# Kernel optimization log

Hardware: AMD Instinct MI355X
Metric: run time of the kernel (lower is better)

## Reference

```python
import jax, jax.numpy as jnp
import numpy as np

V, H, B, NS, SL, QL, AL = 100000, 256, 64, 40, 30, 20, 12
NUM_EPISODE = 3


def setup_inputs() -> dict:
    key = jax.random.key(0)
    ks = iter(jax.random.split(key, 48))
    def p(shape, scale=0.05):
        return jax.random.normal(next(ks), shape, jnp.float32) * scale
    d = {}
    d["c_p"] = jax.random.randint(next(ks), (B, NS, SL), 0, V, dtype=jnp.int32)
    d["c_mask"] = jnp.zeros((B, NS, SL), jnp.int32)
    d["q_p"] = jax.random.randint(next(ks), (B, QL), 0, V, dtype=jnp.int32)
    d["q_mask"] = jnp.zeros((B, QL), jnp.int32)
    d["a_I_p"] = jax.random.randint(next(ks), (B, AL), 0, V, dtype=jnp.int32)
    d["a_I_mask"] = jnp.zeros((B, AL), jnp.int32)
    d["a_II_p"] = jax.random.randint(next(ks), (B, AL), 0, V, dtype=jnp.int32)
    d["a_II_mask"] = jnp.zeros((B, AL), jnp.int32)
    d["embed"] = p((V, H)).at[0].set(0.0)  # padding_idx=0
    for name in ["ctx", "q", "ans", "attn", "mem"]:
        d[name + "_Wih"] = p((3 * H, H))
        d[name + "_Whh"] = p((3 * H, H))
        d[name + "_bih"] = p((3 * H,))
        d[name + "_bhh"] = p((3 * H,))
    d["gate_W1"] = p((H, 7 * H)); d["gate_b1"] = p((H,))
    d["gate_W2"] = p((1, H));     d["gate_b2"] = p((1,))
    d["out_W1"] = p((H, 3 * H)); d["out_b1"] = p((H,))
    d["out_W2"] = p((2, H));     d["out_b2"] = p((2,))
    return d


def _gru_step(h, gi_t, Whh, bhh):
    # PyTorch GRU cell math; gates ordered (r, z, n)
    gh = h @ Whh.T + bhh
    i_r, i_z, i_n = jnp.split(gi_t, 3, -1)
    h_r, h_z, h_n = jnp.split(gh, 3, -1)
    r = jax.nn.sigmoid(i_r + h_r)
    z = jax.nn.sigmoid(i_z + h_z)
    n = jnp.tanh(i_n + r * h_n)
    return (1.0 - z) * n + z * h


def _run_gru(x, Wih, Whh, bih, bhh):
    # x: [N, T, H] -> outputs [N, T, H], zero initial hidden
    gi = jnp.einsum('nth,gh->ntg', x, Wih) + bih  # precompute input projections
    h0 = jnp.zeros((x.shape[0], Whh.shape[1]), x.dtype)
    def step(h, g_t):
        h2 = _gru_step(h, g_t, Whh, bhh)
        return h2, h2
    _, outs = jax.lax.scan(step, h0, jnp.swapaxes(gi, 0, 1))
    return jnp.swapaxes(outs, 0, 1)


def _gather_last(outs, mask):
    # real_length = number of zeros in mask (0 marks a valid token)
    lengths = jnp.sum(mask == 0, axis=-1)
    idx = jnp.clip(lengths - 1, 0, outs.shape[1] - 1)
    return jnp.take_along_axis(outs, idx[:, None, None], axis=1)[:, 0]


def _forward(c_p, c_mask, q_p, q_mask, a_I_p, a_I_mask, a_II_p, a_II_mask,
             embed,
             ctx_Wih, ctx_Whh, ctx_bih, ctx_bhh,
             q_Wih, q_Whh, q_bih, q_bhh,
             ans_Wih, ans_Whh, ans_bih, ans_bhh,
             attn_Wih, attn_Whh, attn_bih, attn_bhh,
             mem_Wih, mem_Whh, mem_bih, mem_bhh,
             gate_W1, gate_b1, gate_W2, gate_b2,
             out_W1, out_b1, out_W2, out_b2):
    b, ns, sl = c_p.shape
    # Context encoding: all (batch, sentence) pairs through one batched GRU
    ce = embed[c_p.reshape(b * ns, sl)]                      # [B*NS, SL, H]
    c_out = _run_gru(ce, ctx_Wih, ctx_Whh, ctx_bih, ctx_bhh)
    enc_ctx = _gather_last(c_out, c_mask.reshape(b * ns, sl)).reshape(b, ns, -1)  # [B, NS, H]
    # Question / answers
    enc_q = _gather_last(_run_gru(embed[q_p], q_Wih, q_Whh, q_bih, q_bhh), q_mask)          # [B, H]
    enc_a1 = _gather_last(_run_gru(embed[a_I_p], ans_Wih, ans_Whh, ans_bih, ans_bhh), a_I_mask)
    enc_a2 = _gather_last(_run_gru(embed[a_II_p], ans_Wih, ans_Whh, ans_bih, ans_bhh), a_II_mask)
    # Episodic memory: gated attention GRU scan over context sentences
    ctx_t = jnp.swapaxes(enc_ctx, 0, 1)  # [NS, B, H]
    memory = enc_q
    for _ in range(NUM_EPISODE):
        mem_now = memory
        def step(h, ct):
            feat = jnp.concatenate([ct, mem_now, enc_q, ct * enc_q, ct * mem_now,
                                    jnp.abs(ct - enc_q), jnp.abs(ct - mem_now)], axis=1)  # [B, 7H]
            g = jax.nn.sigmoid(jnp.tanh(feat @ gate_W1.T + gate_b1) @ gate_W2.T + gate_b2)  # [B, 1]
            hc = _gru_step(h, ct @ attn_Wih.T + attn_bih, attn_Whh, attn_bhh)
            return g * hc + (1.0 - g) * h, None
        e, _ = jax.lax.scan(step, jnp.zeros_like(memory), ctx_t)
        memory = _gru_step(memory, e @ mem_Wih.T + mem_bih, mem_Whh, mem_bhh)
    final = jnp.concatenate([memory, enc_a1, enc_a2], axis=1)  # [B, 3H]
    logits = jnp.tanh(final @ out_W1.T + out_b1) @ out_W2.T + out_b2  # [B, 2]
    return jax.nn.softmax(logits, axis=-1)


def reference(c_p, c_mask, q_p, q_mask, a_I_p, a_I_mask, a_II_p, a_II_mask,
              embed,
              ctx_Wih, ctx_Whh, ctx_bih, ctx_bhh,
              q_Wih, q_Whh, q_bih, q_bhh,
              ans_Wih, ans_Whh, ans_bih, ans_bhh,
              attn_Wih, attn_Whh, attn_bih, attn_bhh,
              mem_Wih, mem_Whh, mem_bih, mem_bhh,
              gate_W1, gate_b1, gate_W2, gate_b2,
              out_W1, out_b1, out_W2, out_b2):
    return _forward(c_p, c_mask, q_p, q_mask, a_I_p, a_I_mask, a_II_p, a_II_mask,
                    embed,
                    ctx_Wih, ctx_Whh, ctx_bih, ctx_bhh,
                    q_Wih, q_Whh, q_bih, q_bhh,
                    ans_Wih, ans_Whh, ans_bih, ans_bhh,
                    attn_Wih, attn_Whh, attn_bih, attn_bhh,
                    mem_Wih, mem_Whh, mem_bih, mem_bhh,
                    gate_W1, gate_b1, gate_W2, gate_b2,
                    out_W1, out_b1, out_W2, out_b2)
```

## Files before the change

### kernel.cpp

```cpp
#include <hip/hip_runtime.h>

typedef unsigned short u16;
typedef __bf16 bf16x8 __attribute__((ext_vector_type(8)));
typedef float f32x4 __attribute__((ext_vector_type(4)));
typedef float f32x4v __attribute__((ext_vector_type(4)));
typedef unsigned int u32x2 __attribute__((ext_vector_type(2)));

#define NSENT 40
#define SLEN 30
#define QLEN 20
#define ALEN 12
#define SCTX 2560
#define SLOT 24
#define TP 12288

__device__ __forceinline__ float b2f(u16 u){ union{float f; unsigned i;} v; v.i = ((unsigned)u)<<16; return v.f; }
__device__ __forceinline__ u16 f2b(float f){ union{float f; unsigned u;} v; v.f=f; unsigned u=v.u; u += ((u>>16)&1u) + 0x7fffu; return (u16)(u>>16); }
__device__ __forceinline__ float sigm(float x){ return __builtin_amdgcn_rcpf(1.f + __expf(-x)); }
__device__ __forceinline__ float tanh_(float x){
  float a = fminf(fmaxf(2.f*x, -30.f), 30.f);
  float e = __expf(a);
  return 1.f - 2.f*__builtin_amdgcn_rcpf(e + 1.f);
}
__device__ __forceinline__ f32x4 mfma16(bf16x8 a, bf16x8 b, f32x4 c){
  return __builtin_amdgcn_mfma_f32_16x16x32_bf16(a, b, c, 0, 0, 0);
}

__global__ void k_prep(
    const float* cWih, const float* cWhh, const float* qWih, const float* qWhh,
    const float* aWih, const float* aWhh, const float* tWih, const float* tWhh,
    const float* mWih, const float* mWhh, const float* gW1,
    const float* cbih, const float* cbhh, const float* qbih, const float* qbhh,
    const float* abih, const float* abhh, const float* tbih, const float* tbhh,
    const float* mbih, const float* mbhh,
    u16* P0,u16* P1,u16* P2,u16* P3,u16* P4,u16* P5,u16* P6,u16* P7,u16* P8,u16* P9,
    u16* PgW1,
    float* B0,float* B1,float* B2,float* B3,float* B4,float* B5,float* B6,float* B7,
    float* B8,float* B9)
{
  int i = blockIdx.x*512 + threadIdx.x;
  if (i < 1966080){
    int seg = i/196608; int e = i - seg*196608;
    int np = e>>8, k = e&255;
    int g16 = np/48, rem = np - g16*48, gate = rem>>4, cc = rem&15;
    int j = gate*256 + g16*16 + cc;
    const float* S; u16* D;
    switch(seg){
      case 0: S=cWih; D=P0; break; case 1: S=cWhh; D=P1; break;
      case 2: S=qWih; D=P2; break; case 3: S=qWhh; D=P3; break;
      case 4: S=aWih; D=P4; break; case 5: S=aWhh; D=P5; break;
      case 6: S=tWih; D=P6; break; case 7: S=tWhh; D=P7; break;
      case 8: S=mWih; D=P8; break; default: S=mWhh; D=P9; break;
    }
    D[e] = f2b(S[j*256 + k]);
  } else if (i < 2424832){
    int e = i - 1966080;
    PgW1[e] = f2b(gW1[e]);
  } else {
    int e = i - 2424832;
    int seg = e/768; int np = e - seg*768;
    int g16 = np/48, rem = np - g16*48, gate = rem>>4, cc = rem&15;
    int j = gate*256 + g16*16 + cc;
    const float* S; float* D;
    switch(seg){
      case 0: S=cbih; D=B0; break; case 1: S=cbhh; D=B1; break;
      case 2: S=qbih; D=B2; break; case 3: S=qbhh; D=B3; break;
      case 4: S=abih; D=B4; break; case 5: S=abhh; D=B5; break;
      case 6: S=tbih; D=B6; break; case 7: S=tbhh; D=B7; break;
      case 8: S=mbih; D=B8; break; default: S=mbhh; D=B9; break;
    }
    D[np] = S[j];
  }
}

__global__ __launch_bounds__(512, 4) void k_xproj(
    const int* c_p, const int* q_p, const int* a1p, const int* a2p,
    const float* embed,
    const u16* cWihP, const u16* qWihP, const u16* aWihP,
    const float* cBih, const float* qBih, const float* aBih,
    u16* gi_c, u16* gi_q, u16* gi_a1, u16* gi_a2)
{
  __shared__ u16 xb[64][288];
  int bid=blockIdx.x, tid=threadIdx.x;
  const int* toks; const u16* W; const float* bias; u16* out; int T, blk32, t0;
  if (bid < 1200){ toks=c_p; W=cWihP; bias=cBih; out=gi_c; T=SLEN; blk32=bid/15; t0=(bid-blk32*15)*2; }
  else if (bid < 1220){ int e=bid-1200; toks=q_p; W=qWihP; bias=qBih; out=gi_q; T=QLEN; blk32=e/10; t0=(e-blk32*10)*2; }
  else if (bid < 1232){ int e=bid-1220; toks=a1p; W=aWihP; bias=aBih; out=gi_a1; T=ALEN; blk32=e/6; t0=(e-blk32*6)*2; }
  else               { int e=bid-1232; toks=a2p; W=aWihP; bias=aBih; out=gi_a2; T=ALEN; blk32=e/6; t0=(e-blk32*6)*2; }
  int seq0 = blk32*32;
  #pragma unroll
  for (int p=0;p<8;p++){
    int i=p*512+tid; int row=i>>6, f4=i&63;
    int tp=row>>5, sm=row&31;
    int tok = toks[(seq0+sm)*T + t0+tp];
    f32x4v v = __builtin_nontemporal_load((const f32x4v*)(embed + (long)tok*256) + f4);
    unsigned lo = (unsigned)f2b(v[0]) | ((unsigned)f2b(v[1])<<16);
    unsigned hi = (unsigned)f2b(v[2]) | ((unsigned)f2b(v[3])<<16);
    u32x2 pk; pk.x=lo; pk.y=hi;
    *(u32x2*)&xb[row][f4*4] = pk;
  }
  const int w=tid>>6, lane=tid&63, c=lane&15, quad=lane>>4;
  __syncthreads();
  #pragma unroll
  for (int jj=0;jj<2;jj++){
    f32x4 acc[4][3];
    #pragma unroll
    for (int Mt=0;Mt<4;Mt++)
      #pragma unroll
      for (int g=0;g<3;g++) acc[Mt][g]=(f32x4){0.f,0.f,0.f,0.f};
    #pragma unroll
    for (int Kt=0;Kt<8;Kt++){
      bf16x8 a0=*(const bf16x8*)&xb[c][Kt*32+quad*8];
      bf16x8 a1=*(const bf16x8*)&xb[16+c][Kt*32+quad*8];
      bf16x8 a2=*(const bf16x8*)&xb[32+c][Kt*32+quad*8];
      bf16x8 a3=*(const bf16x8*)&xb[48+c][Kt*32+quad*8];
      #pragma unroll
      for (int g=0;g<3;g++){
        bf16x8 bfr=*(const bf16x8*)(W + (w*96+(jj*3+g)*16+c)*256 + Kt*32 + quad*8);
        acc[0][g]=mfma16(a0,bfr,acc[0][g]);
        acc[1][g]=mfma16(a1,bfr,acc[1][g]);
        acc[2][g]=mfma16(a2,bfr,acc[2][g]);
        acc[3][g]=mfma16(a3,bfr,acc[3][g]);
      }
    }
    float bv[3];
    #pragma unroll
    for (int g=0;g<3;g++) bv[g]=bias[w*96+(jj*3+g)*16+c];
    #pragma unroll
    for (int Mt=0;Mt<4;Mt++){
      int tp=Mt>>1, smh=Mt&1;
      unsigned d[6];
      #pragma unroll
      for (int k=0;k<6;k++){
        int s0=2*k, s1=2*k+1;
        int r0=s0/3, g0=s0%3, r1=s1/3, g1=s1%3;
        unsigned lo=f2b(acc[Mt][g0][r0]+bv[g0]);
        unsigned hi=f2b(acc[Mt][g1][r1]+bv[g1]);
        d[k]=lo|(hi<<16);
      }
      long block16 = (long)blk32*2 + smh;
      u16* dst = out + (block16*T + t0+tp)*TP + jj*6144 + (w*64+lane)*12;
      u32x2 s0v; s0v.x=d[0]; s0v.y=d[1];
      u32x2 s1v; s1v.x=d[2]; s1v.y=d[3];
      u32x2 s2v; s2v.x=d[4]; s2v.y=d[5];
      __builtin_nontemporal_store(s0v, (u32x2*)dst);
      __builtin_nontemporal_store(s1v, (u32x2*)(dst+4));
      __builtin_nontemporal_store(s2v, (u32x2*)(dst+8));
    }
  }
}

__global__ __launch_bounds__(512, 2) void k_enc_scan(
    const int* c_mask, const int* q_mask, const int* a1m, const int* a2m,
    const u16* cWhhP, const u16* qWhhP, const u16* aWhhP,
    const float* cBhh, const float* qBhh, const float* aBhh,
    const u16* gi_c, const u16* gi_q, const u16* gi_a1, const u16* gi_a2,
    u16* enc_hi, u16* enc_lo, float* enc_qf, float* enc_a1f, float* enc_a2f)
{
  __shared__ u16 hhi[16][264];
  __shared__ u16 hlo[16][264];
  __shared__ int idxs[16];
  int bid=blockIdx.x, tid=threadIdx.x;
  const int* msk; const u16* W; const float* bhh; const u16* gi; int T, seq0, mode;
  u16 *ohi=0, *olo=0; float* of=0;
  if (bid<160){ msk=c_mask; W=cWhhP; bhh=cBhh; gi=gi_c+(long)bid*SLEN*TP; T=SLEN; seq0=bid*16; mode=0; ohi=enc_hi; olo=enc_lo; }
  else if (bid<164){ int e=bid-160; msk=q_mask; W=qWhhP; bhh=qBhh; gi=gi_q+(long)e*QLEN*TP; T=QLEN; seq0=e*16; mode=1; of=enc_qf; }
  else if (bid<168){ int e=bid-164; msk=a1m; W=aWhhP; bhh=aBhh; gi=gi_a1+(long)e*ALEN*TP; T=ALEN; seq0=e*16; mode=1; of=enc_a1f; }
  else             { int e=bid-168; msk=a2m; W=aWhhP; bhh=aBhh; gi=gi_a2+(long)e*ALEN*TP; T=ALEN; seq0=e*16; mode=1; of=enc_a2f; }
  if (tid<16){
    int len=0; const int* mr=msk+(seq0+tid)*T;
    for (int t=0;t<T;t++) len += (mr[t]==0);
    int id=len-1; if(id<0)id=0; if(id>T-1)id=T-1; idxs[tid]=id;
  }
  for (int i=tid;i<16*264;i+=512){ ((u16*)hhi)[i]=0; ((u16*)hlo)[i]=0; }
  const int w=tid>>6, lane=tid&63, c=lane&15, quad=lane>>4;
  float biasv[6];
  #pragma unroll
  for (int nt=0;nt<6;nt++) biasv[nt]=bhh[w*96+nt*16+c];
  uint4 breg[48];
  #pragma unroll
  for (int nt=0;nt<6;nt++)
    #pragma unroll
    for (int Kt=0;Kt<8;Kt++)
      breg[nt*8+Kt] = *(const uint4*)(W + (w*96+nt*16+c)*256 + Kt*32 + quad*8);
  float hreg[8];
  #pragma unroll
  for (int i=0;i<8;i++) hreg[i]=0.f;
  const u16* gp = gi + (w*64+lane)*12;
  u32x2 pA0=*(const u32x2*)(gp),      pA1=*(const u32x2*)(gp+4),    pA2=*(const u32x2*)(gp+8);
  u32x2 pA3=*(const u32x2*)(gp+6144), pA4=*(const u32x2*)(gp+6148), pA5=*(const u32x2*)(gp+6152);
  __syncthreads();
  int idxr[4];
  #pragma unroll
  for (int r=0;r<4;r++) idxr[r]=idxs[quad*4+r];

  for (int t=0;t<T;t++){
    u32x2 pB0,pB1,pB2,pB3,pB4,pB5;
    bool pf=(t+1<T);
    if (pf){
      const u16* gn = gp + (long)(t+1)*TP;
      pB0=*(const u32x2*)(gn);      pB1=*(const u32x2*)(gn+4);    pB2=*(const u32x2*)(gn+8);
      pB3=*(const u32x2*)(gn+6144); pB4=*(const u32x2*)(gn+6148); pB5=*(const u32x2*)(gn+6152);
    }
    f32x4 acc[6];
    #pragma unroll
    for (int nt=0;nt<6;nt++) acc[nt]=(f32x4){0.f,0.f,0.f,0.f};
    #pragma unroll
    for (int Kt=0;Kt<8;Kt++){
      bf16x8 a=*(const bf16x8*)&hhi[c][Kt*32+quad*8];
      #pragma unroll
      for (int nt=0;nt<6;nt++) acc[nt]=mfma16(a,*(const bf16x8*)&breg[nt*8+Kt],acc[nt]);
    }
    #pragma unroll
    for (int Kt=0;Kt<8;Kt++){
      bf16x8 a=*(const bf16x8*)&hlo[c][Kt*32+quad*8];
      #pragma unroll
      for (int nt=0;nt<6;nt++) acc[nt]=mfma16(a,*(const bf16x8*)&breg[nt*8+Kt],acc[nt]);
    }
    unsigned pd[12];
    *(u32x2*)&pd[0]=pA0; *(u32x2*)&pd[2]=pA1; *(u32x2*)&pd[4]=pA2;
    *(u32x2*)&pd[6]=pA3; *(u32x2*)&pd[8]=pA4; *(u32x2*)&pd[10]=pA5;
    #pragma unroll
    for (int r=0;r<4;r++){
      int m=quad*4+r;
      #pragma unroll
      for (int jj=0;jj<2;jj++){
        int j=w*32+jj*16+c;
        int ib=r*3;
        float ir = b2f((u16)((pd[jj*6+(ib>>1)]     >> ((ib&1)*16)) & 0xffffu));
        float iz = b2f((u16)((pd[jj*6+((ib+1)>>1)] >> (((ib+1)&1)*16)) & 0xffffu));
        float in_= b2f((u16)((pd[jj*6+((ib+2)>>1)] >> (((ib+2)&1)*16)) & 0xffffu));
        float hr=acc[jj*3+0][r]+biasv[jj*3+0];
        float hz=acc[jj*3+1][r]+biasv[jj*3+1];
        float hn=acc[jj*3+2][r]+biasv[jj*3+2];
        float rr=sigm(ir+hr), zz=sigm(iz+hz), nn=tanh_(in_+rr*hn);
        float ho=hreg[r*2+jj];
        float hnew=(1.f-zz)*nn+zz*ho;
        hreg[r*2+jj]=hnew;
        u16 hi_=f2b(hnew); u16 lo_=f2b(hnew-b2f(hi_));
        hhi[m][j]=hi_; hlo[m][j]=lo_;
        if (t==idxr[r]){
          long o=(long)(seq0+m)*256+j;
          if (mode==0){ ohi[o]=hi_; olo[o]=lo_; }
          else of[o]=hnew;
        }
      }
    }
    __syncthreads();
    pA0=pB0; pA1=pB1; pA2=pB2; pA3=pB3; pA4=pB4; pA5=pB5;
  }
}

__global__ __launch_bounds__(512, 2) void k_gi(
    const u16* enc_hi, const u16* enc_lo, const u16* tWihP, const float* tBih,
    float* gi_attn, const float* enc_qf, float* mem_f)
{
  int bid=blockIdx.x, tid=threadIdx.x;
  if (bid==160){ for (int i=tid;i<64*256;i+=512) mem_f[i]=enc_qf[i]; return; }
  __shared__ u16 ahi[16][264];
  __shared__ u16 alo[16][264];
  int bblk=bid/40, s=bid-bblk*40, b0=bblk*16;
  {
    int row=tid>>5, ch=tid&31;
    long seq=(long)(b0+row)*NSENT + s;
    *(uint4*)((char*)&ahi[row][0]+ch*16) = *((const uint4*)(enc_hi+seq*256)+ch);
    *(uint4*)((char*)&alo[row][0]+ch*16) = *((const uint4*)(enc_lo+seq*256)+ch);
  }
  const int w=tid>>6, lane=tid&63, c=lane&15, quad=lane>>4;
  f32x4 acc[6];
  #pragma unroll
  for (int nt=0;nt<6;nt++) acc[nt]=(f32x4){0.f,0.f,0.f,0.f};
  __syncthreads();
  #pragma unroll
  for (int Kt=0;Kt<8;Kt++){
    bf16x8 a=*(const bf16x8*)&ahi[c][Kt*32+quad*8];
    #pragma unroll
    for (int nt=0;nt<6;nt++){
      bf16x8 bfr=*(const bf16x8*)(tWihP + (w*96+nt*16+c)*256 + Kt*32 + quad*8);
      acc[nt]=mfma16(a,bfr,acc[nt]);
    }
  }
  #pragma unroll
  for (int Kt=0;Kt<8;Kt++){
    bf16x8 a=*(const bf16x8*)&alo[c][Kt*32+quad*8];
    #pragma unroll
    for (int nt=0;nt<6;nt++){
      bf16x8 bfr=*(const bf16x8*)(tWihP + (w*96+nt*16+c)*256 + Kt*32 + quad*8);
      acc[nt]=mfma16(a,bfr,acc[nt]);
    }
  }
  float biasv[6];
  #pragma unroll
  for (int nt=0;nt<6;nt++) biasv[nt]=tBih[w*96+nt*16+c];
  float* dst = gi_attn + ((long)(bblk*40+s))*TP + (w*64+lane)*SLOT;
  #pragma unroll
  for (int d=0;d<6;d++){
    float4 v;
    #pragma unroll
    for (int e=0;e<4;e++){
      int idx=4*d+e;
      int r=idx/6, rem=idx%6, jj=rem/3, g=rem%3;
      ((float*)&v)[e]=acc[jj*3+g][r]+biasv[jj*3+g];
    }
    *(float4*)(dst+4*d)=v;
  }
}

__global__ __launch_bounds__(512, 1) void k_gatepre(
    const u16* enc_hi, const u16* enc_lo, const float* enc_qf,
    const u16* W1, const float* b1, float* partial)
{
  __shared__ float ctf[32][257];
  __shared__ float qvf[32][257];
  __shared__ u16 ab[32][264];
  int bid=blockIdx.x, tid=threadIdx.x, seq0=bid*32;
  #pragma unroll
  for (int p=0;p<16;p++){
    int i=p*512+tid; int row=i>>8, j=i&255;
    int grow=seq0+row; int b=grow/NSENT;
    ctf[row][j]=b2f(enc_hi[(long)grow*256+j])+b2f(enc_lo[(long)grow*256+j]);
    qvf[row][j]=enc_qf[b*256+j];
  }
  const int w=tid>>6, lane=tid&63, c=lane&15, quad=lane>>4;
  f32x4 acc[2][2];
  #pragma unroll
  for (int nt=0;nt<2;nt++){
    float bv=b1[(w*2+nt)*16+c];
    acc[0][nt]=(f32x4){bv,bv,bv,bv}; acc[1][nt]=acc[0][nt];
  }
  const int chl[4]={0,2,3,5};
  for (int ci=0; ci<4; ci++){
    int ch=chl[ci];
    __syncthreads();
    #pragma unroll
    for (int p=0;p<16;p++){
      int i=p*512+tid; int row=i>>8, j=i&255;
      float ct=ctf[row][j], qv=qvf[row][j];
      float v;
      if      (ch==0) v=ct;
      else if (ch==2) v=qv;
      else if (ch==3) v=ct*qv;
      else            v=fabsf(ct-qv);
      ab[row][j]=f2b(v);
    }
    __syncthreads();
    #pragma unroll
    for (int Kt=0;Kt<8;Kt++){
      bf16x8 a0=*(const bf16x8*)&ab[c][Kt*32+quad*8];
      bf16x8 a1=*(const bf16x8*)&ab[16+c][Kt*32+quad*8];
      #pragma unroll
      for (int nt=0;nt<2;nt++){
        int n=(w*2+nt)*16+c;
        bf16x8 bfr=*(const bf16x8*)(W1 + (long)n*1792 + ch*256 + Kt*32 + quad*8);
        acc[0][nt]=mfma16(a0,bfr,acc[0][nt]);
        acc[1][nt]=mfma16(a1,bfr,acc[1][nt]);
      }
    }
  }
  #pragma unroll
  for (int Mt=0;Mt<2;Mt++)
    #pragma unroll
    for (int nt=0;nt<2;nt++)
      #pragma unroll
      for (int r=0;r<4;r++)
        partial[(long)(seq0+Mt*16+quad*4+r)*256 + (w*2+nt)*16+c] = acc[Mt][nt][r];
}

__global__ __launch_bounds__(512, 1) void k_gate(
    const u16* enc_hi, const u16* enc_lo, const float* mem_f,
    const float* partial, const u16* W1, const float* W2, const float* b2v, float* g)
{
  __shared__ float ctf[32][257];
  __shared__ float mvf[32][257];
  __shared__ u16 ab[32][264];
  __shared__ float pl[32][8];
  int bid=blockIdx.x, tid=threadIdx.x, seq0=bid*32;
  #pragma unroll
  for (int p=0;p<16;p++){
    int i=p*512+tid; int row=i>>8, j=i&255;
    int grow=seq0+row; int b=grow/NSENT;
    ctf[row][j]=b2f(enc_hi[(long)grow*256+j])+b2f(enc_lo[(long)grow*256+j]);
    mvf[row][j]=mem_f[b*256+j];
  }
  const int w=tid>>6, lane=tid&63, c=lane&15, quad=lane>>4;
  f32x4 acc[2][2];
  float w2v[2];
  #pragma unroll
  for (int nt=0;nt<2;nt++){
    int n=(w*2+nt)*16+c;
    w2v[nt]=W2[n];
    #pragma unroll
    for (int Mt=0;Mt<2;Mt++)
      #pragma unroll
      for (int r=0;r<4;r++)
        acc[Mt][nt][r]=partial[(long)(seq0+Mt*16+quad*4+r)*256 + n];
  }
  const int chl[3]={1,4,6};
  for (int ci=0; ci<3; ci++){
    int ch=chl[ci];
    __syncthreads();
    #pragma unroll
    for (int p=0;p<16;p++){
      int i=p*512+tid; int row=i>>8, j=i&255;
      float ct=ctf[row][j], mv=mvf[row][j];
      float v;
      if      (ch==1) v=mv;
      else if (ch==4) v=ct*mv;
      else            v=fabsf(ct-mv);
      ab[row][j]=f2b(v);
    }
    __syncthreads();
    #pragma unroll
    for (int Kt=0;Kt<8;Kt++){
      bf16x8 a0=*(const bf16x8*)&ab[c][Kt*32+quad*8];
      bf16x8 a1=*(const bf16x8*)&ab[16+c][Kt*32+quad*8];
      #pragma unroll
      for (int nt=0;nt<2;nt++){
        int n=(w*2+nt)*16+c;
        bf16x8 bfr=*(const bf16x8*)(W1 + (long)n*1792 + ch*256 + Kt*32 + quad*8);
        acc[0][nt]=mfma16(a0,bfr,acc[0][nt]);
        acc[1][nt]=mfma16(a1,bfr,acc[1][nt]);
      }
    }
  }
  float pm[8];
  #pragma unroll
  for (int i=0;i<8;i++){
    int Mt=i>>2, r=i&3;
    float s=0.f;
    #pragma unroll
    for (int nt=0;nt<2;nt++) s += tanh_(acc[Mt][nt][r])*w2v[nt];
    pm[i]=s;
  }
  #pragma unroll
  for (int off=1;off<16;off<<=1)
    #pragma unroll
    for (int i=0;i<8;i++) pm[i]+=__shfl_xor(pm[i],off,64);
  if (c==0){
    #pragma unroll
    for (int i=0;i<8;i++){ int m=(i>>2)*16+quad*4+(i&3); pl[m][w]=pm[i]; }
  }
  __syncthreads();
  if (tid<32){
    float s=b2v[0];
    #pragma unroll
    for (int ww=0;ww<8;ww++) s+=pl[tid][ww];
    g[seq0+tid]=sigm(s);
  }
}

__global__ __launch_bounds__(512, 2) void k_scan(
    const u16* tWhhP, const float* tBhh,
    const float* gi_attn, const float* g,
    float* mem_f, const u16* mWihP, const u16* mWhhP,
    const float* mBih, const float* mBhh)
{
  __shared__ u16 hb[16][264];
  __shared__ u16 mhi[16][264];
  __shared__ u16 mlo[16][264];
  __shared__ float memfl[16][256];
  __shared__ float gl[16][40];
  int bid=blockIdx.x, tid=threadIdx.x, b0=bid*16;
  const int w=tid>>6, lane=tid&63, c=lane&15, quad=lane>>4;
  for (int i=tid;i<16*264;i+=512){ ((u16*)hb)[i]=0; }
  for (int i=tid;i<4096;i+=512){
    int m=i>>8, j=i&255;
    float v=mem_f[(b0+m)*256+j]; memfl[m][j]=v;
    u16 hi_=f2b(v); mhi[m][j]=hi_; mlo[m][j]=f2b(v-b2f(hi_));
  }
  for (int i=tid;i<640;i+=512){ int m=i/40, s=i-m*40; gl[m][s]=g[(b0+m)*40+s]; }
  float biasv[6];
  #pragma unroll
  for (int nt=0;nt<6;nt++) biasv[nt]=tBhh[w*96+nt*16+c];
  uint4 breg[48];
  #pragma unroll
  for (int nt=0;nt<6;nt++)
    #pragma unroll
    for (int Kt=0;Kt<8;Kt++)
      breg[nt*8+Kt] = *(const uint4*)(tWhhP + (w*96+nt*16+c)*256 + Kt*32 + quad*8);
  float hreg[8];
  #pragma unroll
  for (int i=0;i<8;i++) hreg[i]=0.f;
  const float* gp = gi_attn + ((long)bid*NSENT)*TP + (w*64+lane)*SLOT;
  float4 pA[6];
  #pragma unroll
  for (int d=0;d<6;d++) pA[d]=*(const float4*)(gp+4*d);
  __syncthreads();

  for (int s=0;s<NSENT;s++){
    float4 pB[6];
    bool pf=(s+1<NSENT);
    if (pf){
      const float* gn = gp + (long)(s+1)*TP;
      #pragma unroll
      for (int d=0;d<6;d++) pB[d]=*(const float4*)(gn+4*d);
    }
    f32x4 acc[6];
    #pragma unroll
    for (int nt=0;nt<6;nt++) acc[nt]=(f32x4){0.f,0.f,0.f,0.f};
    #pragma unroll
    for (int Kt=0;Kt<8;Kt++){
      bf16x8 a=*(const bf16x8*)&hb[c][Kt*32+quad*8];
      #pragma unroll
      for (int nt=0;nt<6;nt++) acc[nt]=mfma16(a,*(const bf16x8*)&breg[nt*8+Kt],acc[nt]);
    }
    const float* pf32 = (const float*)&pA[0];
    #pragma unroll
    for (int r=0;r<4;r++){
      int m=quad*4+r;
      float gv = gl[m][s];
      #pragma unroll
      for (int jj=0;jj<2;jj++){
        int j=w*32+jj*16+c;
        int ib=(r*2+jj)*3;
        float ir=pf32[ib], iz=pf32[ib+1], in_=pf32[ib+2];
        float hr=acc[jj*3+0][r]+biasv[jj*3+0];
        float hz=acc[jj*3+1][r]+biasv[jj*3+1];
        float hn=acc[jj*3+2][r]+biasv[jj*3+2];
        float rr=sigm(ir+hr), zz=sigm(iz+hz), nn=tanh_(in_+rr*hn);
        float ho=hreg[r*2+jj];
        float hc=(1.f-zz)*nn+zz*ho;
        float hnew=gv*hc+(1.f-gv)*ho;
        hreg[r*2+jj]=hnew;
        hb[m][j]=f2b(hnew);
      }
    }
    __syncthreads();
    #pragma unroll
    for (int d=0;d<6;d++) pA[d]=pB[d];
  }
  f32x4 ai[6], ah[6];
  #pragma unroll
  for (int nt=0;nt<6;nt++){ ai[nt]=(f32x4){0.f,0.f,0.f,0.f}; ah[nt]=ai[nt]; }
  #pragma unroll
  for (int Kt=0;Kt<8;Kt++){
    bf16x8 a=*(const bf16x8*)&hb[c][Kt*32+quad*8];
    #pragma unroll
    for (int nt=0;nt<6;nt++){
      bf16x8 bfr=*(const bf16x8*)(mWihP + (w*96+nt*16+c)*256 + Kt*32 + quad*8);
      ai[nt]=mfma16(a,bfr,ai[nt]);
    }
  }
  #pragma unroll
  for (int Kt=0;Kt<8;Kt++){
    bf16x8 a=*(const bf16x8*)&mhi[c][Kt*32+quad*8];
    #pragma unroll
    for (int nt=0;nt<6;nt++){
      bf16x8 bfr=*(const bf16x8*)(mWhhP + (w*96+nt*16+c)*256 + Kt*32 + quad*8);
      ah[nt]=mfma16(a,bfr,ah[nt]);
    }
  }
  #pragma unroll
  for (int Kt=0;Kt<8;Kt++){
    bf16x8 a=*(const bf16x8*)&mlo[c][Kt*32+quad*8];
    #pragma unroll
    for (int nt=0;nt<6;nt++){
      bf16x8 bfr=*(const bf16x8*)(mWhhP + (w*96+nt*16+c)*256 + Kt*32 + quad*8);
      ah[nt]=mfma16(a,bfr,ah[nt]);
    }
  }
  float bih6[6], bhh6[6];
  #pragma unroll
  for (int nt=0;nt<6;nt++){ bih6[nt]=mBih[w*96+nt*16+c]; bhh6[nt]=mBhh[w*96+nt*16+c]; }
  #pragma unroll
  for (int r=0;r<4;r++){
    int m=quad*4+r;
    #pragma unroll
    for (int jj=0;jj<2;jj++){
      int j=w*32+jj*16+c;
      float ir=ai[jj*3+0][r]+bih6[jj*3+0];
      float iz=ai[jj*3+1][r]+bih6[jj*3+1];
      float in_=ai[jj*3+2][r]+bih6[jj*3+2];
      float hr=ah[jj*3+0][r]+bhh6[jj*3+0];
      float hz=ah[jj*3+1][r]+bhh6[jj*3+1];
      float hn=ah[jj*3+2][r]+bhh6[jj*3+2];
      float rr=sigm(ir+hr), zz=sigm(iz+hz), nn=tanh_(in_+rr*hn);
      float mo=memfl[m][j];
      mem_f[(b0+m)*256+j]=(1.f-zz)*nn+zz*mo;
    }
  }
}

__global__ void k_final(const float* mem_f, const float* a1f, const float* a2f,
    const float* W1o, const float* b1o, const float* W2o, const float* b2o, float* outp)
{
  __shared__ float af[768];
  __shared__ float tl[256];
  __shared__ float lg[2];
  int b=blockIdx.x, tid=threadIdx.x;
  af[tid]     = mem_f[b*256+tid];
  af[256+tid] = a1f[b*256+tid];
  af[512+tid] = a2f[b*256+tid];
  __syncthreads();
  float s=b1o[tid];
  const float* wr=W1o + (long)tid*768;
  for (int k=0;k<768;k++) s += af[k]*wr[k];
  tl[tid]=tanh_(s);
  __syncthreads();
  if (tid<2){
    float l=b2o[tid];
    const float* w2=W2o + tid*256;
    for (int k=0;k<256;k++) l += tl[k]*w2[k];
    lg[tid]=l;
  }
  __syncthreads();
  if (tid==0){
    float m=fmaxf(lg[0],lg[1]);
    float e0=__expf(lg[0]-m), e1=__expf(lg[1]-m);
    float inv=1.f/(e0+e1);
    outp[b*2]=e0*inv; outp[b*2+1]=e1*inv;
  }
}

extern "C" void kernel_launch(void* const* d_in, const int* in_sizes, int n_in,
                              void* d_out, int out_size, void* d_ws, size_t ws_size,
                              hipStream_t stream) {
  const int* c_p   = (const int*)d_in[0];
  const int* c_m   = (const int*)d_in[1];
  const int* q_p   = (const int*)d_in[2];
  const int* q_m   = (const int*)d_in[3];
  const int* a1p   = (const int*)d_in[4];
  const int* a1m   = (const int*)d_in[5];
  const int* a2p   = (const int*)d_in[6];
  const int* a2m   = (const int*)d_in[7];
  const float* embed = (const float*)d_in[8];
  const float* cWih=(const float*)d_in[9],  *cWhh=(const float*)d_in[10], *cbih=(const float*)d_in[11], *cbhh=(const float*)d_in[12];
  const float* qWih=(const float*)d_in[13], *qWhh=(const float*)d_in[14], *qbih=(const float*)d_in[15], *qbhh=(const float*)d_in[16];
  const float* aWih=(const float*)d_in[17], *aWhh=(const float*)d_in[18], *abih=(const float*)d_in[19], *abhh=(const float*)d_in[20];
  const float* tWih=(const float*)d_in[21], *tWhh=(const float*)d_in[22], *tbih=(const float*)d_in[23], *tbhh=(const float*)d_in[24];
  const float* mWih=(const float*)d_in[25], *mWhh=(const float*)d_in[26], *mbih=(const float*)d_in[27], *mbhh=(const float*)d_in[28];
  const float* gW1=(const float*)d_in[29], *gb1=(const float*)d_in[30], *gW2=(const float*)d_in[31], *gb2=(const float*)d_in[32];
  const float* oW1=(const float*)d_in[33], *ob1=(const float*)d_in[34], *oW2=(const float*)d_in[35], *ob2=(const float*)d_in[36];

  char* ws = (char*)d_ws;
  size_t off = 0;
  u16* P[10];
  for (int i=0;i<10;i++){ P[i]=(u16*)(ws+off); off+=393216; }
  u16* PgW1 =(u16*)(ws+off); off+=917504;
  float* B[10];
  for (int i=0;i<10;i++){ B[i]=(float*)(ws+off); off+=3072; }
  u16* gi_c =(u16*)(ws+off); off+=(size_t)160*SLEN*TP*2;
  u16* gi_q =(u16*)(ws+off); off+=(size_t)4*QLEN*TP*2;
  u16* gi_a1=(u16*)(ws+off); off+=(size_t)4*ALEN*TP*2;
  u16* gi_a2=(u16*)(ws+off); off+=(size_t)4*ALEN*TP*2;
  u16* enc_hi=(u16*)(ws+off); off+=(size_t)SCTX*256*2;
  u16* enc_lo=(u16*)(ws+off); off+=(size_t)SCTX*256*2;
  float* enc_qf =(float*)(ws+off); off+=64*256*4;
  float* enc_a1f=(float*)(ws+off); off+=64*256*4;
  float* enc_a2f=(float*)(ws+off); off+=64*256*4;
  float* mem_f  =(float*)(ws+off); off+=64*256*4;
  float* gi_attn=(float*)(ws+off); off+=(size_t)160*TP*4;
  float* partial=(float*)(ws+off); off+=(size_t)SCTX*256*4;
  float* gbuf   =(float*)(ws+off); off+=SCTX*4;

  k_prep<<<4751, 512, 0, stream>>>(cWih,cWhh,qWih,qWhh,aWih,aWhh,tWih,tWhh,mWih,mWhh,gW1,
      cbih,cbhh,qbih,qbhh,abih,abhh,tbih,tbhh,mbih,mbhh,
      P[0],P[1],P[2],P[3],P[4],P[5],P[6],P[7],P[8],P[9], PgW1,
      B[0],B[1],B[2],B[3],B[4],B[5],B[6],B[7],B[8],B[9]);

  k_xproj<<<1244, 512, 0, stream>>>(c_p,q_p,a1p,a2p, embed,
      P[0],P[2],P[4], B[0],B[2],B[4], gi_c,gi_q,gi_a1,gi_a2);

  k_enc_scan<<<172, 512, 0, stream>>>(c_m,q_m,a1m,a2m,
      P[1],P[3],P[5], B[1],B[3],B[5], gi_c,gi_q,gi_a1,gi_a2,
      enc_hi,enc_lo, enc_qf,enc_a1f,enc_a2f);

  k_gi<<<161, 512, 0, stream>>>(enc_hi,enc_lo, P[6], B[6], gi_attn, enc_qf, mem_f);

  k_gatepre<<<80, 512, 0, stream>>>(enc_hi,enc_lo, enc_qf, PgW1, gb1, partial);

  for (int ep=0; ep<3; ep++){
    k_gate<<<80, 512, 0, stream>>>(enc_hi,enc_lo, mem_f, partial, PgW1, gW2, gb2, gbuf);
    k_scan<<<4, 512, 0, stream>>>(P[7], B[7], gi_attn, gbuf, mem_f, P[8], P[9], B[8], B[9]);
  }

  k_final<<<64, 256, 0, stream>>>(mem_f, enc_a1f, enc_a2f, oW1, ob1, oW2, ob2, (float*)d_out);
}
```

Before: 893.6 us.

## Trim register-resident GRU weights and drop prefetch in scan kernels

```diff
diff --git a/kernel.cpp b/kernel.cpp
--- a/kernel.cpp
+++ b/kernel.cpp
@@ -150,7 +150,7 @@
   }
 }
 
-__global__ __launch_bounds__(512, 2) void k_enc_scan(
+__global__ __launch_bounds__(512, 1) void k_enc_scan(
     const int* c_mask, const int* q_mask, const int* a1m, const int* a2m,
     const u16* cWhhP, const u16* qWhhP, const u16* aWhhP,
     const float* cBhh, const float* qBhh, const float* aBhh,
@@ -177,12 +177,14 @@
   float biasv[6];
   #pragma unroll
   for (int nt=0;nt<6;nt++) biasv[nt]=bhh[w*96+nt*16+c];
-  uint4 breg[48];
-  #pragma unroll
-  for (int nt=0;nt<6;nt++)
+  uint4 breg[32];
+  #pragma unroll
+  for (int nt=0;nt<4;nt++)
     #pragma unroll
     for (int Kt=0;Kt<8;Kt++)
       breg[nt*8+Kt] = *(const uint4*)(W + (w*96+nt*16+c)*256 + Kt*32 + quad*8);
+  const u16* W4 = W + (w*96+64+c)*256 + quad*8;
+  const u16* W5 = W + (w*96+80+c)*256 + quad*8;
   float hreg[8];
   #pragma unroll
   for (int i=0;i<8;i++) hreg[i]=0.f;
@@ -207,15 +209,17 @@
     for (int nt=0;nt<6;nt++) acc[nt]=(f32x4){0.f,0.f,0.f,0.f};
     #pragma unroll
     for (int Kt=0;Kt<8;Kt++){
-      bf16x8 a=*(const bf16x8*)&hhi[c][Kt*32+quad*8];
-      #pragma unroll
-      for (int nt=0;nt<6;nt++) acc[nt]=mfma16(a,*(const bf16x8*)&breg[nt*8+Kt],acc[nt]);
-    }
-    #pragma unroll
-    for (int Kt=0;Kt<8;Kt++){
-      bf16x8 a=*(const bf16x8*)&hlo[c][Kt*32+quad*8];
-      #pragma unroll
-      for (int nt=0;nt<6;nt++) acc[nt]=mfma16(a,*(const bf16x8*)&breg[nt*8+Kt],acc[nt]);
+      bf16x8 ahi_=*(const bf16x8*)&hhi[c][Kt*32+quad*8];
+      bf16x8 alo_=*(const bf16x8*)&hlo[c][Kt*32+quad*8];
+      bf16x8 b4=*(const bf16x8*)(W4 + Kt*32);
+      bf16x8 b5=*(const bf16x8*)(W5 + Kt*32);
+      #pragma unroll
+      for (int nt=0;nt<4;nt++){
+        acc[nt]=mfma16(ahi_,*(const bf16x8*)&breg[nt*8+Kt],acc[nt]);
+        acc[nt]=mfma16(alo_,*(const bf16x8*)&breg[nt*8+Kt],acc[nt]);
+      }
+      acc[4]=mfma16(ahi_,b4,acc[4]); acc[4]=mfma16(alo_,b4,acc[4]);
+      acc[5]=mfma16(ahi_,b5,acc[5]); acc[5]=mfma16(alo_,b5,acc[5]);
     }
     unsigned pd[12];
     *(u32x2*)&pd[0]=pA0; *(u32x2*)&pd[2]=pA1; *(u32x2*)&pd[4]=pA2;
@@ -449,7 +453,7 @@
   }
 }
 
-__global__ __launch_bounds__(512, 2) void k_scan(
+__global__ __launch_bounds__(512, 1) void k_scan(
     const u16* tWhhP, const float* tBhh,
     const float* gi_attn, const float* g,
     float* mem_f, const u16* mWihP, const u16* mWhhP,
@@ -472,12 +476,14 @@
   float biasv[6];
   #pragma unroll
   for (int nt=0;nt<6;nt++) biasv[nt]=tBhh[w*96+nt*16+c];
-  uint4 breg[48];
-  #pragma unroll
-  for (int nt=0;nt<6;nt++)
+  uint4 breg[32];
+  #pragma unroll
+  for (int nt=0;nt<4;nt++)
     #pragma unroll
     for (int Kt=0;Kt<8;Kt++)
       breg[nt*8+Kt] = *(const uint4*)(tWhhP + (w*96+nt*16+c)*256 + Kt*32 + quad*8);
+  const u16* W4 = tWhhP + (w*96+64+c)*256 + quad*8;
+  const u16* W5 = tWhhP + (w*96+80+c)*256 + quad*8;
   float hreg[8];
   #pragma unroll
   for (int i=0;i<8;i++) hreg[i]=0.f;
@@ -488,21 +494,18 @@
   __syncthreads();
 
   for (int s=0;s<NSENT;s++){
-    float4 pB[6];
-    bool pf=(s+1<NSENT);
-    if (pf){
-      const float* gn = gp + (long)(s+1)*TP;
-      #pragma unroll
-      for (int d=0;d<6;d++) pB[d]=*(const float4*)(gn+4*d);
-    }
     f32x4 acc[6];
     #pragma unroll
     for (int nt=0;nt<6;nt++) acc[nt]=(f32x4){0.f,0.f,0.f,0.f};
     #pragma unroll
     for (int Kt=0;Kt<8;Kt++){
       bf16x8 a=*(const bf16x8*)&hb[c][Kt*32+quad*8];
-      #pragma unroll
-      for (int nt=0;nt<6;nt++) acc[nt]=mfma16(a,*(const bf16x8*)&breg[nt*8+Kt],acc[nt]);
+      bf16x8 b4=*(const bf16x8*)(W4 + Kt*32);
+      bf16x8 b5=*(const bf16x8*)(W5 + Kt*32);
+      #pragma unroll
+      for (int nt=0;nt<4;nt++) acc[nt]=mfma16(a,*(const bf16x8*)&breg[nt*8+Kt],acc[nt]);
+      acc[4]=mfma16(a,b4,acc[4]);
+      acc[5]=mfma16(a,b5,acc[5]);
     }
     const float* pf32 = (const float*)&pA[0];
     #pragma unroll
@@ -526,8 +529,11 @@
       }
     }
     __syncthreads();
-    #pragma unroll
-    for (int d=0;d<6;d++) pA[d]=pB[d];
+    if (s+1<NSENT){
+      const float* gn = gp + (long)(s+1)*TP;
+      #pragma unroll
+      for (int d=0;d<6;d++) pA[d]=*(const float4*)(gn+4*d);
+    }
   }
   f32x4 ai[6], ah[6];
   #pragma unroll
```

Result: slower. 1.272 ms (+42.3%).

## Split gate kernels across output-column halves with atomic partial reduction

Applied to the files above, without the earlier changes.

```diff
diff --git a/kernel.cpp b/kernel.cpp
--- a/kernel.cpp
+++ b/kernel.cpp
@@ -313,7 +313,8 @@
   __shared__ float ctf[32][257];
   __shared__ float qvf[32][257];
   __shared__ u16 ab[32][264];
-  int bid=blockIdx.x, tid=threadIdx.x, seq0=bid*32;
+  int bid=blockIdx.x, tid=threadIdx.x;
+  int seqgrp=bid>>1, nh=bid&1, seq0=seqgrp*32;
   #pragma unroll
   for (int p=0;p<16;p++){
     int i=p*512+tid; int row=i>>8, j=i&255;
@@ -322,11 +323,11 @@
     qvf[row][j]=enc_qf[b*256+j];
   }
   const int w=tid>>6, lane=tid&63, c=lane&15, quad=lane>>4;
-  f32x4 acc[2][2];
-  #pragma unroll
-  for (int nt=0;nt<2;nt++){
-    float bv=b1[(w*2+nt)*16+c];
-    acc[0][nt]=(f32x4){bv,bv,bv,bv}; acc[1][nt]=acc[0][nt];
+  const int n = nh*128 + w*16 + c;
+  f32x4 acc[2];
+  {
+    float bv=b1[n];
+    acc[0]=(f32x4){bv,bv,bv,bv}; acc[1]=acc[0];
   }
   const int chl[4]={0,2,3,5};
   for (int ci=0; ci<4; ci++){
@@ -348,33 +349,28 @@
     for (int Kt=0;Kt<8;Kt++){
       bf16x8 a0=*(const bf16x8*)&ab[c][Kt*32+quad*8];
       bf16x8 a1=*(const bf16x8*)&ab[16+c][Kt*32+quad*8];
-      #pragma unroll
-      for (int nt=0;nt<2;nt++){
-        int n=(w*2+nt)*16+c;
-        bf16x8 bfr=*(const bf16x8*)(W1 + (long)n*1792 + ch*256 + Kt*32 + quad*8);
-        acc[0][nt]=mfma16(a0,bfr,acc[0][nt]);
-        acc[1][nt]=mfma16(a1,bfr,acc[1][nt]);
-      }
+      bf16x8 bfr=*(const bf16x8*)(W1 + (long)n*1792 + ch*256 + Kt*32 + quad*8);
+      acc[0]=mfma16(a0,bfr,acc[0]);
+      acc[1]=mfma16(a1,bfr,acc[1]);
     }
   }
   #pragma unroll
   for (int Mt=0;Mt<2;Mt++)
     #pragma unroll
-    for (int nt=0;nt<2;nt++)
-      #pragma unroll
-      for (int r=0;r<4;r++)
-        partial[(long)(seq0+Mt*16+quad*4+r)*256 + (w*2+nt)*16+c] = acc[Mt][nt][r];
+    for (int r=0;r<4;r++)
+      partial[(long)(seq0+Mt*16+quad*4+r)*256 + n] = acc[Mt][r];
 }
 
 __global__ __launch_bounds__(512, 1) void k_gate(
     const u16* enc_hi, const u16* enc_lo, const float* mem_f,
-    const float* partial, const u16* W1, const float* W2, const float* b2v, float* g)
+    const float* partial, const u16* W1, const float* W2, float* g)
 {
   __shared__ float ctf[32][257];
   __shared__ float mvf[32][257];
   __shared__ u16 ab[32][264];
   __shared__ float pl[32][8];
-  int bid=blockIdx.x, tid=threadIdx.x, seq0=bid*32;
+  int bid=blockIdx.x, tid=threadIdx.x;
+  int seqgrp=bid>>1, nh=bid&1, seq0=seqgrp*32;
   #pragma unroll
   for (int p=0;p<16;p++){
     int i=p*512+tid; int row=i>>8, j=i&255;
@@ -383,18 +379,14 @@
     mvf[row][j]=mem_f[b*256+j];
   }
   const int w=tid>>6, lane=tid&63, c=lane&15, quad=lane>>4;
-  f32x4 acc[2][2];
-  float w2v[2];
-  #pragma unroll
-  for (int nt=0;nt<2;nt++){
-    int n=(w*2+nt)*16+c;
-    w2v[nt]=W2[n];
-    #pragma unroll
-    for (int Mt=0;Mt<2;Mt++)
-      #pragma unroll
-      for (int r=0;r<4;r++)
-        acc[Mt][nt][r]=partial[(long)(seq0+Mt*16+quad*4+r)*256 + n];
-  }
+  const int n = nh*128 + w*16 + c;
+  f32x4 acc[2];
+  float w2v=W2[n];
+  #pragma unroll
+  for (int Mt=0;Mt<2;Mt++)
+    #pragma unroll
+    for (int r=0;r<4;r++)
+      acc[Mt][r]=partial[(long)(seq0+Mt*16+quad*4+r)*256 + n];
   const int chl[3]={1,4,6};
   for (int ci=0; ci<3; ci++){
     int ch=chl[ci];
@@ -414,23 +406,16 @@
     for (int Kt=0;Kt<8;Kt++){
       bf16x8 a0=*(const bf16x8*)&ab[c][Kt*32+quad*8];
       bf16x8 a1=*(const bf16x8*)&ab[16+c][Kt*32+quad*8];
-      #pragma unroll
-      for (int nt=0;nt<2;nt++){
-        int n=(w*2+nt)*16+c;
-        bf16x8 bfr=*(const bf16x8*)(W1 + (long)n*1792 + ch*256 + Kt*32 + quad*8);
-        acc[0][nt]=mfma16(a0,bfr,acc[0][nt]);
-        acc[1][nt]=mfma16(a1,bfr,acc[1][nt]);
-      }
+      bf16x8 bfr=*(const bf16x8*)(W1 + (long)n*1792 + ch*256 + Kt*32 + quad*8);
+      acc[0]=mfma16(a0,bfr,acc[0]);
+      acc[1]=mfma16(a1,bfr,acc[1]);
     }
   }
   float pm[8];
   #pragma unroll
   for (int i=0;i<8;i++){
     int Mt=i>>2, r=i&3;
-    float s=0.f;
-    #pragma unroll
-    for (int nt=0;nt<2;nt++) s += tanh_(acc[Mt][nt][r])*w2v[nt];
-    pm[i]=s;
+    pm[i]=tanh_(acc[Mt][r])*w2v;
   }
   #pragma unroll
   for (int off=1;off<16;off<<=1)
@@ -442,16 +427,16 @@
   }
   __syncthreads();
   if (tid<32){
-    float s=b2v[0];
+    float s=0.f;
     #pragma unroll
     for (int ww=0;ww<8;ww++) s+=pl[tid][ww];
-    g[seq0+tid]=sigm(s);
+    atomicAdd(&g[seq0+tid], s);
   }
 }
 
 __global__ __launch_bounds__(512, 2) void k_scan(
     const u16* tWhhP, const float* tBhh,
-    const float* gi_attn, const float* g,
+    const float* gi_attn, const float* g, const float* gb2,
     float* mem_f, const u16* mWihP, const u16* mWhhP,
     const float* mBih, const float* mBhh)
 {
@@ -468,7 +453,10 @@
     float v=mem_f[(b0+m)*256+j]; memfl[m][j]=v;
     u16 hi_=f2b(v); mhi[m][j]=hi_; mlo[m][j]=f2b(v-b2f(hi_));
   }
-  for (int i=tid;i<640;i+=512){ int m=i/40, s=i-m*40; gl[m][s]=g[(b0+m)*40+s]; }
+  {
+    float b2s = gb2[0];
+    for (int i=tid;i<640;i+=512){ int m=i/40, s=i-m*40; gl[m][s]=sigm(g[(b0+m)*40+s]+b2s); }
+  }
   float biasv[6];
   #pragma unroll
   for (int nt=0;nt<6;nt++) biasv[nt]=tBhh[w*96+nt*16+c];
@@ -667,11 +655,12 @@
 
   k_gi<<<161, 512, 0, stream>>>(enc_hi,enc_lo, P[6], B[6], gi_attn, enc_qf, mem_f);
 
-  k_gatepre<<<80, 512, 0, stream>>>(enc_hi,enc_lo, enc_qf, PgW1, gb1, partial);
+  k_gatepre<<<160, 512, 0, stream>>>(enc_hi,enc_lo, enc_qf, PgW1, gb1, partial);
 
   for (int ep=0; ep<3; ep++){
-    k_gate<<<80, 512, 0, stream>>>(enc_hi,enc_lo, mem_f, partial, PgW1, gW2, gb2, gbuf);
-    k_scan<<<4, 512, 0, stream>>>(P[7], B[7], gi_attn, gbuf, mem_f, P[8], P[9], B[8], B[9]);
+    hipMemsetAsync(gbuf, 0, SCTX*4, stream);
+    k_gate<<<160, 512, 0, stream>>>(enc_hi,enc_lo, mem_f, partial, PgW1, gW2, gbuf);
+    k_scan<<<4, 512, 0, stream>>>(P[7], B[7], gi_attn, gbuf, gb2, mem_f, P[8], P[9], B[8], B[9]);
   }
 
   k_final<<<64, 256, 0, stream>>>(mem_f, enc_a1f, enc_a2f, oW1, ob1, oW2, ob2, (float*)d_out);
```

Measured after the change: 878.1 us. About the same (-1.7%).
